# Performance work log

Measured on AMD Instinct MI355X. Metric: run time of the kernel, lower is better.

Reference implementation:

```python
import jax, jax.numpy as jnp
import numpy as np

V, H_BASE, D, L, K = 32000, 4096, 512, 2, 4
B = 64

def setup_inputs() -> dict:
    key = jax.random.key(0)
    ks = jax.random.split(key, 12)
    s = 0.02
    return {
        "hidden_state": jax.random.normal(ks[0], (B, H_BASE), jnp.float32),
        "in_proj_w": jax.random.normal(ks[1], (D, H_BASE), jnp.float32) * s,
        "in_proj_b": jnp.zeros((D,), jnp.float32),
        "w_ih0": jax.random.normal(ks[2], (3 * D, D), jnp.float32) * s,
        "w_hh0": jax.random.normal(ks[3], (3 * D, D), jnp.float32) * s,
        "b_ih0": jax.random.normal(ks[4], (3 * D,), jnp.float32) * s,
        "b_hh0": jax.random.normal(ks[5], (3 * D,), jnp.float32) * s,
        "w_ih1": jax.random.normal(ks[6], (3 * D, D), jnp.float32) * s,
        "w_hh1": jax.random.normal(ks[7], (3 * D, D), jnp.float32) * s,
        "b_ih1": jax.random.normal(ks[8], (3 * D,), jnp.float32) * s,
        "b_hh1": jax.random.normal(ks[9], (3 * D,), jnp.float32) * s,
        "embed": jax.random.normal(ks[10], (V, D), jnp.float32) * s,
        "out_w": jax.random.normal(ks[11], (V, D), jnp.float32) * s,
    }

def _gru_cell(x, h, w_ih, w_hh, b_ih, b_hh):
    # PyTorch GRU gate order: r, z, n
    gi = x @ w_ih.T + b_ih  # [B, 3D]
    gh = h @ w_hh.T + b_hh
    ir, iz, inn = jnp.split(gi, 3, axis=-1)
    hr, hz, hn = jnp.split(gh, 3, axis=-1)
    r = jax.nn.sigmoid(ir + hr)
    z = jax.nn.sigmoid(iz + hz)
    n = jnp.tanh(inn + r * hn)
    return (1.0 - z) * n + z * h

def reference(hidden_state, in_proj_w, in_proj_b, w_ih0, w_hh0, b_ih0, b_hh0,
              w_ih1, w_hh1, b_ih1, b_hh1, embed, out_w):
    b = hidden_state.shape[0]
    h0 = hidden_state @ in_proj_w.T + in_proj_b  # [B, D]
    h_l0 = h0
    h_l1 = h0
    x = jnp.zeros((b, in_proj_w.shape[0]), hidden_state.dtype)
    all_logits = []
    for _ in range(K):
        h_l0 = _gru_cell(x, h_l0, w_ih0, w_hh0, b_ih0, b_hh0)
        h_l1 = _gru_cell(h_l0, h_l1, w_ih1, w_hh1, b_ih1, b_hh1)
        logits = h_l1 @ out_w.T  # [B, V]
        all_logits.append(logits)
        x = embed[jnp.argmax(logits, axis=-1)]  # greedy next-token embed
    return jnp.stack(all_logits, axis=1)  # [B, K, V]
```

## Files before the change

kernel.cpp:

```cpp
#include <hip/hip_runtime.h>
#include <math.h>


typedef __attribute__((ext_vector_type(8))) short short8;
typedef __attribute__((ext_vector_type(4))) float f32x4;

__device__ __forceinline__ unsigned short f2bf_rne(float x) {
    unsigned u = __float_as_uint(x);
    unsigned r = (u + 0x7fffu + ((u >> 16) & 1u)) >> 16;
    return (unsigned short)r;
}
__device__ __forceinline__ void split2(float x, unsigned short& hi, unsigned short& lo) {
    unsigned u = __float_as_uint(x);
    hi = (unsigned short)(u >> 16);
    float r = x - __uint_as_float(u & 0xffff0000u);
    lo = f2bf_rne(r);
}

__device__ __forceinline__ void store_plane(unsigned short* hiP, unsigned short* loP,
                                            int m, int d, float v) {
    int s = d >> 6, cl = (d >> 3) & 7, e = d & 7;
    int off = m * 512 + s * 64 + ((cl ^ (m & 7)) * 8) + e;
    unsigned short hi, lo; split2(v, hi, lo);
    hiP[off] = hi; loP[off] = lo;
}

__device__ __forceinline__ void gload16(const void* g, void* lds) {
    __builtin_amdgcn_global_load_lds(
        (const __attribute__((address_space(1))) unsigned int*)g,
        (__attribute__((address_space(3))) unsigned int*)lds, 16, 0, 0);
}

__device__ __forceinline__ void split_w_body(
    const float* __restrict__ W, unsigned short* __restrict__ H,
    unsigned short* __restrict__ L, size_t g, int kclog)
{
    int n  = (int)(g >> kclog);
    int c8 = (int)g & ((1 << kclog) - 1);
    const float* src = W + g * 8;
    float4 v0 = *(const float4*)src;
    float4 v1 = *(const float4*)(src + 4);
    unsigned short h[8], l[8];
    split2(v0.x,h[0],l[0]); split2(v0.y,h[1],l[1]); split2(v0.z,h[2],l[2]); split2(v0.w,h[3],l[3]);
    split2(v1.x,h[4],l[4]); split2(v1.y,h[5],l[5]); split2(v1.z,h[6],l[6]); split2(v1.w,h[7],l[7]);
    uint4 ph = make_uint4((unsigned)h[0]|((unsigned)h[1]<<16), (unsigned)h[2]|((unsigned)h[3]<<16),
                          (unsigned)h[4]|((unsigned)h[5]<<16), (unsigned)h[6]|((unsigned)h[7]<<16));
    uint4 pl = make_uint4((unsigned)l[0]|((unsigned)l[1]<<16), (unsigned)l[2]|((unsigned)l[3]<<16),
                          (unsigned)l[4]|((unsigned)l[5]<<16), (unsigned)l[6]|((unsigned)l[7]<<16));
    int nt = n >> 7, row = n & 127;
    int ksi = c8 >> 3;
    int slot = (c8 & 7) ^ (row & 7);
    int tpr = 1 << (kclog - 3);
    size_t off = ((size_t)(nt * tpr + ksi) * 128 + row) * 64 + slot * 8;
    *(uint4*)(H + off) = ph;
    *(uint4*)(L + off) = pl;
}

__global__ __launch_bounds__(256) void k_split_W(
    const float* __restrict__ W, unsigned short* __restrict__ H,
    unsigned short* __restrict__ L, int kclog)
{
    size_t g = (size_t)blockIdx.x * 256 + threadIdx.x;
    split_w_body(W, H, L, g, kclog);
}

__global__ __launch_bounds__(256) void k_split_gw(
    const float* __restrict__ w0, const float* __restrict__ w1,
    const float* __restrict__ w2, const float* __restrict__ w3,
    unsigned short* __restrict__ H, unsigned short* __restrict__ L)
{
    int mat = blockIdx.y;
    const float* W = mat == 0 ? w0 : mat == 1 ? w1 : mat == 2 ? w2 : w3;
    size_t g = (size_t)blockIdx.x * 256 + threadIdx.x;
    split_w_body(W, H + (size_t)mat * 786432, L + (size_t)mat * 786432, g, 6);
}

template<bool ARGMAX>
__device__ __forceinline__ void mfma_gemm(
    const char* __restrict__ AH, const char* __restrict__ AL, int AstrideB, int akk0,
    const unsigned short* __restrict__ BH, const unsigned short* __restrict__ BL,
    size_t btileU,
    int nk,
    float* __restrict__ C, int ldc, int n0,
    unsigned short (*AsH)[4096], unsigned short (*AsL)[4096],
    unsigned short (*BsH)[8192], unsigned short (*BsL)[8192],
    float* __restrict__ pval, int* __restrict__ pidx, int bx)
{
    const int tid  = threadIdx.x;
    const int wv   = tid >> 6;
    const int lane = tid & 63;
    const int lr   = lane & 15;
    const int lh   = lane >> 4;
    const int m    = tid >> 3;
    const int cp   = tid & 7;

    f32x4 acc[4];
#pragma unroll
    for (int i = 0; i < 4; ++i) acc[i] = (f32x4){0.f, 0.f, 0.f, 0.f};

    auto stage = [&](int t, int p) {
        const int ka = (akk0 + t * 64) * 2;
        gload16(AH + m * AstrideB + ka + cp * 16, (char*)AsH[p] + wv * 1024);
        gload16(AL + m * AstrideB + ka + cp * 16, (char*)AsL[p] + wv * 1024);
        const char* bH = (const char*)BH + (btileU + (size_t)t * 8192) * 2;
        const char* bL = (const char*)BL + (btileU + (size_t)t * 8192) * 2;
        gload16(bH + wv * 2048 +        lane * 16, (char*)BsH[p] + wv * 2048);
        gload16(bH + wv * 2048 + 1024 + lane * 16, (char*)BsH[p] + wv * 2048 + 1024);
        gload16(bL + wv * 2048 +        lane * 16, (char*)BsL[p] + wv * 2048);
        gload16(bL + wv * 2048 + 1024 + lane * 16, (char*)BsL[p] + wv * 2048 + 1024);
    };

    stage(0, 0);
    __syncthreads();

    for (int t = 0; t < nk; ++t) {
        const int p = t & 1;
        if (t + 1 < nk) stage(t + 1, p ^ 1);
#pragma unroll
        for (int kk2 = 0; kk2 < 2; ++kk2) {
            int aoff = lr * 64 + (((kk2 * 4 + lh) ^ (lr & 7)) * 8);
            short8 ah[4], al[4];
#pragma unroll
            for (int mt = 0; mt < 4; ++mt) {
                ah[mt] = *(const short8*)(AsH[p] + mt * 1024 + aoff);
                al[mt] = *(const short8*)(AsL[p] + mt * 1024 + aoff);
            }
            int brow = wv * 16 + lr;
            int boff = brow * 64 + (((kk2 * 4 + lh) ^ (brow & 7)) * 8);
            short8 bh = *(const short8*)(BsH[p] + boff);
            short8 bl = *(const short8*)(BsL[p] + boff);
#pragma unroll
            for (int mt = 0; mt < 4; ++mt) {
                acc[mt] = __builtin_amdgcn_mfma_f32_16x16x32_bf16(ah[mt], bh, acc[mt], 0, 0, 0);
                acc[mt] = __builtin_amdgcn_mfma_f32_16x16x32_bf16(ah[mt], bl, acc[mt], 0, 0, 0);
                acc[mt] = __builtin_amdgcn_mfma_f32_16x16x32_bf16(al[mt], bh, acc[mt], 0, 0, 0);
            }
        }
        __syncthreads();
    }

#pragma unroll
    for (int mt = 0; mt < 4; ++mt)
#pragma unroll
        for (int i = 0; i < 4; ++i) {
            int mm = mt * 16 + lh * 4 + i;
            C[mm * ldc + n0 + wv * 16 + lr] = acc[mt][i];
        }

    if (ARGMAX) {
        float* sv = (float*)&AsH[0][0];
        int*   sc = (int*)&AsL[0][0];
#pragma unroll
        for (int mt = 0; mt < 4; ++mt)
#pragma unroll
            for (int i = 0; i < 4; ++i) {
                float v = acc[mt][i];
                int   c = n0 + wv * 16 + lr;
#pragma unroll
                for (int msk = 1; msk < 16; msk <<= 1) {
                    float ov = __shfl_xor(v, msk, 64);
                    int   oc = __shfl_xor(c, msk, 64);
                    if (ov > v || (ov == v && oc < c)) { v = ov; c = oc; }
                }
                if (lr == 0) {
                    int row = mt * 16 + lh * 4 + i;
                    sv[wv * 64 + row] = v;
                    sc[wv * 64 + row] = c;
                }
            }
        __syncthreads();
        if (tid < 64) {
            float v = sv[tid]; int c = sc[tid];
#pragma unroll
            for (int w = 1; w < 8; ++w) {
                float ov = sv[w * 64 + tid]; int oc = sc[w * 64 + tid];
                if (ov > v) { v = ov; c = oc; }
            }
            pval[bx * 64 + tid] = v;
            pidx[bx * 64 + tid] = c;
        }
    }
}

#define DECLARE_LDS() \
    __shared__ alignas(16) unsigned short AsH[2][4096]; \
    __shared__ alignas(16) unsigned short AsL[2][4096]; \
    __shared__ alignas(16) unsigned short BsH[2][8192]; \
    __shared__ alignas(16) unsigned short BsL[2][8192];

__global__ __launch_bounds__(256) void k_split_A(
    const float* __restrict__ hidden, char* __restrict__ hidH, char* __restrict__ hidL)
{
    int g = blockIdx.x * 256 + threadIdx.x;
    int m = g >> 9;
    int cc = g & 511;
    int s = cc >> 3, cl = cc & 7;
    const float* src = hidden + m * 4096 + cc * 8;
    float4 v0 = *(const float4*)src;
    float4 v1 = *(const float4*)(src + 4);
    unsigned short h[8], l[8];
    split2(v0.x,h[0],l[0]); split2(v0.y,h[1],l[1]); split2(v0.z,h[2],l[2]); split2(v0.w,h[3],l[3]);
    split2(v1.x,h[4],l[4]); split2(v1.y,h[5],l[5]); split2(v1.z,h[6],l[6]); split2(v1.w,h[7],l[7]);
    uint4 ph = make_uint4((unsigned)h[0]|((unsigned)h[1]<<16), (unsigned)h[2]|((unsigned)h[3]<<16),
                          (unsigned)h[4]|((unsigned)h[5]<<16), (unsigned)h[6]|((unsigned)h[7]<<16));
    uint4 pl = make_uint4((unsigned)l[0]|((unsigned)l[1]<<16), (unsigned)l[2]|((unsigned)l[3]<<16),
                          (unsigned)l[4]|((unsigned)l[5]<<16), (unsigned)l[6]|((unsigned)l[7]<<16));
    int off = m * 8192 + s * 128 + ((cl ^ (m & 7)) * 16);
    *(uint4*)(hidH + off) = ph;
    *(uint4*)(hidL + off) = pl;
}

__global__ __launch_bounds__(512) void k_inproj(
    const char* __restrict__ hidH, const char* __restrict__ hidL,
    const unsigned short* __restrict__ WH, const unsigned short* __restrict__ WL,
    float* __restrict__ part)
{
    DECLARE_LDS();
    int nt = blockIdx.x & 3;
    int ks = blockIdx.x >> 2;
    mfma_gemm<false>(hidH, hidL, 8192, ks * 256,
                     WH, WL, (size_t)(nt * 64 + ks * 4) * 8192, 4,
                     part + ks * 32768, 512, nt * 128,
                     AsH, AsL, BsH, BsL, nullptr, nullptr, 0);
}

__global__ __launch_bounds__(256) void k_reduce_inproj(
    const float* __restrict__ part, const float* __restrict__ bias,
    float* __restrict__ hA, float* __restrict__ hB,
    unsigned short* hAH, unsigned short* hAL,
    unsigned short* hBH, unsigned short* hBL,
    unsigned short* xH,  unsigned short* xL)
{
    int i = blockIdx.x * 256 + threadIdx.x;
    int b = i >> 9;
    int d = i & 511;
    float s = bias[d];
#pragma unroll
    for (int ks = 0; ks < 16; ++ks) s += part[ks * 32768 + i];
    hA[i] = s;
    hB[i] = s;
    store_plane(hAH, hAL, b, d, s);
    store_plane(hBH, hBL, b, d, s);
    store_plane(xH,  xL,  b, d, 0.f);
}

__global__ __launch_bounds__(512) void k_gates(
    const char* __restrict__ xH, const char* __restrict__ xL,
    const char* __restrict__ hH, const char* __restrict__ hL,
    const unsigned short* __restrict__ gwH, const unsigned short* __restrict__ gwL,
    int layer, float* __restrict__ gip, float* __restrict__ ghp)
{
    DECLARE_LDS();
    int bx  = blockIdx.x;
    int nt  = bx % 12;
    int ks  = (bx / 12) & 3;
    int mat = bx / 48;
    const char* AH = mat ? hH : xH;
    const char* AL = mat ? hL : xL;
    float* C = (mat ? ghp : gip) + ks * 98304;
    size_t btile = ((size_t)(layer * 2 + mat) * 96 + nt * 8 + ks * 2) * 8192;
    mfma_gemm<false>(AH, AL, 1024, ks * 128,
                     gwH, gwL, btile, 2,
                     C, 1536, nt * 128,
                     AsH, AsL, BsH, BsL, nullptr, nullptr, 0);
}

__global__ __launch_bounds__(256) void k_combine(
    const float* __restrict__ gip, const float* __restrict__ ghp,
    const float* __restrict__ b_ih, const float* __restrict__ b_hh,
    float* __restrict__ h, unsigned short* hH, unsigned short* hL)
{
    int i = blockIdx.x * 256 + threadIdx.x;
    int b = i >> 9;
    int d = i & 511;
    int base = b * 1536 + d;
    float ir = b_ih[d], iz = b_ih[d + 512], inn = b_ih[d + 1024];
    float hr = b_hh[d], hz = b_hh[d + 512], hn = b_hh[d + 1024];
#pragma unroll
    for (int ks = 0; ks < 4; ++ks) {
        const float* gi = gip + ks * 98304 + base;
        const float* gh = ghp + ks * 98304 + base;
        ir  += gi[0];    iz += gi[512];  inn += gi[1024];
        hr  += gh[0];    hz += gh[512];  hn  += gh[1024];
    }
    float r = 1.f / (1.f + expf(-(ir + hr)));
    float z = 1.f / (1.f + expf(-(iz + hz)));
    float n = tanhf(inn + r * hn);
    float hv = (1.f - z) * n + z * h[i];
    h[i] = hv;
    store_plane(hH, hL, b, d, hv);
}

__global__ __launch_bounds__(512) void k_logits(
    const char* __restrict__ hH, const char* __restrict__ hL,
    const unsigned short* __restrict__ WH, const unsigned short* __restrict__ WL,
    float* __restrict__ out, int step,
    float* __restrict__ pval, int* __restrict__ pidx)
{
    DECLARE_LDS();
    mfma_gemm<true>(hH, hL, 1024, 0,
                    WH, WL, (size_t)blockIdx.x * 8 * 8192, 8,
                    out + step * 32000, 128000, blockIdx.x * 128,
                    AsH, AsL, BsH, BsL, pval, pidx, blockIdx.x);
}

__global__ __launch_bounds__(256) void k_reduce_embed(
    const float* __restrict__ pval, const int* __restrict__ pidx,
    const float* __restrict__ embed, unsigned short* xH, unsigned short* xL)
{
    __shared__ float sv[256];
    __shared__ int   sc[256];
    const int b = blockIdx.x;
    const int tid = threadIdx.x;
    float v = -3.4e38f;
    int   c = 0x7fffffff;
    if (tid < 250) { v = pval[tid * 64 + b]; c = pidx[tid * 64 + b]; }
    sv[tid] = v; sc[tid] = c;
    __syncthreads();
    for (int s = 128; s > 0; s >>= 1) {
        if (tid < s) {
            float ov = sv[tid + s]; int oc = sc[tid + s];
            if (ov > sv[tid] || (ov == sv[tid] && oc < sc[tid])) { sv[tid] = ov; sc[tid] = oc; }
        }
        __syncthreads();
    }
    int tok = sc[0];
    for (int j = tid; j < 512; j += 256)
        store_plane(xH, xL, b, j, embed[tok * 512 + j]);
}

extern "C" void kernel_launch(void* const* d_in, const int* in_sizes, int n_in,
                              void* d_out, int out_size, void* d_ws, size_t ws_size,
                              hipStream_t stream)
{
    const float* hidden = (const float*)d_in[0];
    const float* in_w   = (const float*)d_in[1];
    const float* in_b   = (const float*)d_in[2];
    const float* w_ih0  = (const float*)d_in[3];
    const float* w_hh0  = (const float*)d_in[4];
    const float* b_ih0  = (const float*)d_in[5];
    const float* b_hh0  = (const float*)d_in[6];
    const float* w_ih1  = (const float*)d_in[7];
    const float* w_hh1  = (const float*)d_in[8];
    const float* b_ih1  = (const float*)d_in[9];
    const float* b_hh1  = (const float*)d_in[10];
    const float* embed  = (const float*)d_in[11];
    const float* out_w  = (const float*)d_in[12];
    float* out = (float*)d_out;
    char*  ws  = (char*)d_ws;

    float* hA  = (float*)(ws + 0);
    float* hB  = (float*)(ws + 131072);
    unsigned short* xH  = (unsigned short*)(ws + 262144);
    unsigned short* xL  = (unsigned short*)(ws + 327680);
    unsigned short* hAH = (unsigned short*)(ws + 393216);
    unsigned short* hAL = (unsigned short*)(ws + 458752);
    unsigned short* hBH = (unsigned short*)(ws + 524288);
    unsigned short* hBL = (unsigned short*)(ws + 589824);
    char* hidH = ws + 655360;
    char* hidL = ws + 1179648;
    float* gip = (float*)(ws + 1703936);
    float* ghp = (float*)(ws + 3276800);
    float* pval = (float*)(ws + 4849664);
    int*   pidx = (int*)  (ws + 4913664);
    float* ipart = (float*)(ws + 4980736);
    unsigned short* owH = (unsigned short*)(ws + 8388608);
    unsigned short* owL = (unsigned short*)(ws + 41943040);
    unsigned short* gwH = (unsigned short*)(ws + 75497472);
    unsigned short* gwL = (unsigned short*)(ws + 83886080);
    unsigned short* inH = (unsigned short*)(ws + 92274688);
    unsigned short* inL = (unsigned short*)(ws + 96468992);

    k_split_A<<<128, 256, 0, stream>>>(hidden, hidH, hidL);
    k_split_W<<<8000, 256, 0, stream>>>(out_w, owH, owL, 6);
    k_split_gw<<<dim3(384, 4), 256, 0, stream>>>(w_ih0, w_hh0, w_ih1, w_hh1, gwH, gwL);
    k_split_W<<<1024, 256, 0, stream>>>(in_w, inH, inL, 9);
    k_inproj<<<64, 512, 0, stream>>>(hidH, hidL, inH, inL, ipart);
    k_reduce_inproj<<<128, 256, 0, stream>>>(ipart, in_b, hA, hB,
                                             hAH, hAL, hBH, hBL, xH, xL);

    for (int step = 0; step < 4; ++step) {
        k_gates<<<96, 512, 0, stream>>>((char*)xH, (char*)xL, (char*)hAH, (char*)hAL,
                                        gwH, gwL, 0, gip, ghp);
        k_combine<<<128, 256, 0, stream>>>(gip, ghp, b_ih0, b_hh0, hA, hAH, hAL);
        k_gates<<<96, 512, 0, stream>>>((char*)hAH, (char*)hAL, (char*)hBH, (char*)hBL,
                                        gwH, gwL, 1, gip, ghp);
        k_combine<<<128, 256, 0, stream>>>(gip, ghp, b_ih1, b_hh1, hB, hBH, hBL);
        k_logits<<<250, 512, 0, stream>>>((char*)hBH, (char*)hBL, owH, owL,
                                          out, step, pval, pidx);
        k_reduce_embed<<<64, 256, 0, stream>>>(pval, pidx, embed, xH, xL);
    }
}
```

Before: 361.9 us.

## Fuse out_w hi/lo bf16 split into logits GEMM and drop pre-split pass

The separate kernel that split the 32000x512 fp32 out_w into bf16 hi/lo planes in workspace is removed. The logits kernel now loads fp32 out_w rows directly, splits them in registers and writes swizzled hi/lo tiles into LDS, prefetching the next tile while the current one is multiplied. Tiles shrink to 64 columns with 256 threads and 500 blocks, and the argmax partial reduction and reduce_embed are adapted to 500 partials. This removes the large write and re-read of the split planes, at the cost of repeating the split arithmetic in each of the four steps and reading fp32 (wider) weights per step.

```diff
diff --git a/kernel.cpp b/kernel.cpp
--- a/kernel.cpp
+++ b/kernel.cpp
@@ -75,119 +75,6 @@
     split_w_body(W, H + (size_t)mat * 786432, L + (size_t)mat * 786432, g, 6);
 }
 
-template<bool ARGMAX>
-__device__ __forceinline__ void mfma_gemm(
-    const char* __restrict__ AH, const char* __restrict__ AL, int AstrideB, int akk0,
-    const unsigned short* __restrict__ BH, const unsigned short* __restrict__ BL,
-    size_t btileU,
-    int nk,
-    float* __restrict__ C, int ldc, int n0,
-    unsigned short (*AsH)[4096], unsigned short (*AsL)[4096],
-    unsigned short (*BsH)[8192], unsigned short (*BsL)[8192],
-    float* __restrict__ pval, int* __restrict__ pidx, int bx)
-{
-    const int tid  = threadIdx.x;
-    const int wv   = tid >> 6;
-    const int lane = tid & 63;
-    const int lr   = lane & 15;
-    const int lh   = lane >> 4;
-    const int m    = tid >> 3;
-    const int cp   = tid & 7;
-
-    f32x4 acc[4];
-#pragma unroll
-    for (int i = 0; i < 4; ++i) acc[i] = (f32x4){0.f, 0.f, 0.f, 0.f};
-
-    auto stage = [&](int t, int p) {
-        const int ka = (akk0 + t * 64) * 2;
-        gload16(AH + m * AstrideB + ka + cp * 16, (char*)AsH[p] + wv * 1024);
-        gload16(AL + m * AstrideB + ka + cp * 16, (char*)AsL[p] + wv * 1024);
-        const char* bH = (const char*)BH + (btileU + (size_t)t * 8192) * 2;
-        const char* bL = (const char*)BL + (btileU + (size_t)t * 8192) * 2;
-        gload16(bH + wv * 2048 +        lane * 16, (char*)BsH[p] + wv * 2048);
-        gload16(bH + wv * 2048 + 1024 + lane * 16, (char*)BsH[p] + wv * 2048 + 1024);
-        gload16(bL + wv * 2048 +        lane * 16, (char*)BsL[p] + wv * 2048);
-        gload16(bL + wv * 2048 + 1024 + lane * 16, (char*)BsL[p] + wv * 2048 + 1024);
-    };
-
-    stage(0, 0);
-    __syncthreads();
-
-    for (int t = 0; t < nk; ++t) {
-        const int p = t & 1;
-        if (t + 1 < nk) stage(t + 1, p ^ 1);
-#pragma unroll
-        for (int kk2 = 0; kk2 < 2; ++kk2) {
-            int aoff = lr * 64 + (((kk2 * 4 + lh) ^ (lr & 7)) * 8);
-            short8 ah[4], al[4];
-#pragma unroll
-            for (int mt = 0; mt < 4; ++mt) {
-                ah[mt] = *(const short8*)(AsH[p] + mt * 1024 + aoff);
-                al[mt] = *(const short8*)(AsL[p] + mt * 1024 + aoff);
-            }
-            int brow = wv * 16 + lr;
-            int boff = brow * 64 + (((kk2 * 4 + lh) ^ (brow & 7)) * 8);
-            short8 bh = *(const short8*)(BsH[p] + boff);
-            short8 bl = *(const short8*)(BsL[p] + boff);
-#pragma unroll
-            for (int mt = 0; mt < 4; ++mt) {
-                acc[mt] = __builtin_amdgcn_mfma_f32_16x16x32_bf16(ah[mt], bh, acc[mt], 0, 0, 0);
-                acc[mt] = __builtin_amdgcn_mfma_f32_16x16x32_bf16(ah[mt], bl, acc[mt], 0, 0, 0);
-                acc[mt] = __builtin_amdgcn_mfma_f32_16x16x32_bf16(al[mt], bh, acc[mt], 0, 0, 0);
-            }
-        }
-        __syncthreads();
-    }
-
-#pragma unroll
-    for (int mt = 0; mt < 4; ++mt)
-#pragma unroll
-        for (int i = 0; i < 4; ++i) {
-            int mm = mt * 16 + lh * 4 + i;
-            C[mm * ldc + n0 + wv * 16 + lr] = acc[mt][i];
-        }
-
-    if (ARGMAX) {
-        float* sv = (float*)&AsH[0][0];
-        int*   sc = (int*)&AsL[0][0];
-#pragma unroll
-        for (int mt = 0; mt < 4; ++mt)
-#pragma unroll
-            for (int i = 0; i < 4; ++i) {
-                float v = acc[mt][i];
-                int   c = n0 + wv * 16 + lr;
-#pragma unroll
-                for (int msk = 1; msk < 16; msk <<= 1) {
-                    float ov = __shfl_xor(v, msk, 64);
-                    int   oc = __shfl_xor(c, msk, 64);
-                    if (ov > v || (ov == v && oc < c)) { v = ov; c = oc; }
-                }
-                if (lr == 0) {
-                    int row = mt * 16 + lh * 4 + i;
-                    sv[wv * 64 + row] = v;
-                    sc[wv * 64 + row] = c;
-                }
-            }
-        __syncthreads();
-        if (tid < 64) {
-            float v = sv[tid]; int c = sc[tid];
-#pragma unroll
-            for (int w = 1; w < 8; ++w) {
-                float ov = sv[w * 64 + tid]; int oc = sc[w * 64 + tid];
-                if (ov > v) { v = ov; c = oc; }
-            }
-            pval[bx * 64 + tid] = v;
-            pidx[bx * 64 + tid] = c;
-        }
-    }
-}
-
-#define DECLARE_LDS() \
-    __shared__ alignas(16) unsigned short AsH[2][4096]; \
-    __shared__ alignas(16) unsigned short AsL[2][4096]; \
-    __shared__ alignas(16) unsigned short BsH[2][8192]; \
-    __shared__ alignas(16) unsigned short BsL[2][8192];
-
 __global__ __launch_bounds__(256) void k_split_A(
     const float* __restrict__ hidden, char* __restrict__ hidH, char* __restrict__ hidL)
 {
@@ -210,6 +97,96 @@
     *(uint4*)(hidL + off) = pl;
 }
 
+__device__ __forceinline__ void mfma_core(
+    const unsigned short* __restrict__ AsH0, const unsigned short* __restrict__ AsL0,
+    const unsigned short* __restrict__ BsH0, const unsigned short* __restrict__ BsL0,
+    int wv, int lr, int lh, f32x4* acc)
+{
+#pragma unroll
+    for (int kk2 = 0; kk2 < 2; ++kk2) {
+        int aoff = lr * 64 + (((kk2 * 4 + lh) ^ (lr & 7)) * 8);
+        short8 ah[4], al[4];
+#pragma unroll
+        for (int mt = 0; mt < 4; ++mt) {
+            ah[mt] = *(const short8*)(AsH0 + mt * 1024 + aoff);
+            al[mt] = *(const short8*)(AsL0 + mt * 1024 + aoff);
+        }
+        int brow = wv * 16 + lr;
+        int boff = brow * 64 + (((kk2 * 4 + lh) ^ (brow & 7)) * 8);
+        short8 bh = *(const short8*)(BsH0 + boff);
+        short8 bl = *(const short8*)(BsL0 + boff);
+#pragma unroll
+        for (int mt = 0; mt < 4; ++mt) {
+            acc[mt] = __builtin_amdgcn_mfma_f32_16x16x32_bf16(ah[mt], bh, acc[mt], 0, 0, 0);
+            acc[mt] = __builtin_amdgcn_mfma_f32_16x16x32_bf16(ah[mt], bl, acc[mt], 0, 0, 0);
+            acc[mt] = __builtin_amdgcn_mfma_f32_16x16x32_bf16(al[mt], bh, acc[mt], 0, 0, 0);
+        }
+    }
+}
+
+__device__ __forceinline__ void epilogue_write(
+    float* __restrict__ C, int ldc, int n0, int wv, int lr, int lh, const f32x4* acc)
+{
+#pragma unroll
+    for (int mt = 0; mt < 4; ++mt)
+#pragma unroll
+        for (int i = 0; i < 4; ++i) {
+            int mm = mt * 16 + lh * 4 + i;
+            C[mm * ldc + n0 + wv * 16 + lr] = acc[mt][i];
+        }
+}
+
+__device__ __forceinline__ void mfma_gemm(
+    const char* __restrict__ AH, const char* __restrict__ AL, int AstrideB, int akk0,
+    const unsigned short* __restrict__ BH, const unsigned short* __restrict__ BL,
+    size_t btileU, int nk,
+    float* __restrict__ C, int ldc, int n0,
+    unsigned short (*AsH)[4096], unsigned short (*AsL)[4096],
+    unsigned short (*BsH)[8192], unsigned short (*BsL)[8192])
+{
+    const int tid  = threadIdx.x;
+    const int wv   = tid >> 6;
+    const int lane = tid & 63;
+    const int lr   = lane & 15;
+    const int lh   = lane >> 4;
+    const int m    = tid >> 3;
+    const int cp   = tid & 7;
+
+    f32x4 acc[4];
+#pragma unroll
+    for (int i = 0; i < 4; ++i) acc[i] = (f32x4){0.f, 0.f, 0.f, 0.f};
+
+    auto stage = [&](int t, int p) {
+        const int ka = (akk0 + t * 64) * 2;
+        gload16(AH + m * AstrideB + ka + cp * 16, (char*)AsH[p] + wv * 1024);
+        gload16(AL + m * AstrideB + ka + cp * 16, (char*)AsL[p] + wv * 1024);
+        const char* bH = (const char*)BH + (btileU + (size_t)t * 8192) * 2;
+        const char* bL = (const char*)BL + (btileU + (size_t)t * 8192) * 2;
+        gload16(bH + wv * 2048 +        lane * 16, (char*)BsH[p] + wv * 2048);
+        gload16(bH + wv * 2048 + 1024 + lane * 16, (char*)BsH[p] + wv * 2048 + 1024);
+        gload16(bL + wv * 2048 +        lane * 16, (char*)BsL[p] + wv * 2048);
+        gload16(bL + wv * 2048 + 1024 + lane * 16, (char*)BsL[p] + wv * 2048 + 1024);
+    };
+
+    stage(0, 0);
+    __syncthreads();
+
+    for (int t = 0; t < nk; ++t) {
+        const int p = t & 1;
+        if (t + 1 < nk) stage(t + 1, p ^ 1);
+        mfma_core(AsH[p], AsL[p], BsH[p], BsL[p], wv, lr, lh, acc);
+        __syncthreads();
+    }
+
+    epilogue_write(C, ldc, n0, wv, lr, lh, acc);
+}
+
+#define DECLARE_LDS() \
+    __shared__ alignas(16) unsigned short AsH[2][4096]; \
+    __shared__ alignas(16) unsigned short AsL[2][4096]; \
+    __shared__ alignas(16) unsigned short BsH[2][8192]; \
+    __shared__ alignas(16) unsigned short BsL[2][8192];
+
 __global__ __launch_bounds__(512) void k_inproj(
     const char* __restrict__ hidH, const char* __restrict__ hidL,
     const unsigned short* __restrict__ WH, const unsigned short* __restrict__ WL,
@@ -218,10 +195,10 @@
     DECLARE_LDS();
     int nt = blockIdx.x & 3;
     int ks = blockIdx.x >> 2;
-    mfma_gemm<false>(hidH, hidL, 8192, ks * 256,
-                     WH, WL, (size_t)(nt * 64 + ks * 4) * 8192, 4,
-                     part + ks * 32768, 512, nt * 128,
-                     AsH, AsL, BsH, BsL, nullptr, nullptr, 0);
+    mfma_gemm(hidH, hidL, 8192, ks * 256,
+              WH, WL, (size_t)(nt * 64 + ks * 4) * 8192, 4,
+              part + ks * 32768, 512, nt * 128,
+              AsH, AsL, BsH, BsL);
 }
 
 __global__ __launch_bounds__(256) void k_reduce_inproj(
@@ -259,10 +236,10 @@
     const char* AL = mat ? hL : xL;
     float* C = (mat ? ghp : gip) + ks * 98304;
     size_t btile = ((size_t)(layer * 2 + mat) * 96 + nt * 8 + ks * 2) * 8192;
-    mfma_gemm<false>(AH, AL, 1024, ks * 128,
-                     gwH, gwL, btile, 2,
-                     C, 1536, nt * 128,
-                     AsH, AsL, BsH, BsL, nullptr, nullptr, 0);
+    mfma_gemm(AH, AL, 1024, ks * 128,
+              gwH, gwL, btile, 2,
+              C, 1536, nt * 128,
+              AsH, AsL, BsH, BsL);
 }
 
 __global__ __launch_bounds__(256) void k_combine(
@@ -291,17 +268,115 @@
     store_plane(hH, hL, b, d, hv);
 }
 
-__global__ __launch_bounds__(512) void k_logits(
-    const char* __restrict__ hH, const char* __restrict__ hL,
-    const unsigned short* __restrict__ WH, const unsigned short* __restrict__ WL,
+__global__ __launch_bounds__(256) void k_logits(
+    const char* __restrict__ hBH, const char* __restrict__ hBL,
+    const float* __restrict__ out_w,
     float* __restrict__ out, int step,
     float* __restrict__ pval, int* __restrict__ pidx)
 {
-    DECLARE_LDS();
-    mfma_gemm<true>(hH, hL, 1024, 0,
-                    WH, WL, (size_t)blockIdx.x * 8 * 8192, 8,
-                    out + step * 32000, 128000, blockIdx.x * 128,
-                    AsH, AsL, BsH, BsL, pval, pidx, blockIdx.x);
+    __shared__ alignas(16) unsigned short AsH[2][4096];
+    __shared__ alignas(16) unsigned short AsL[2][4096];
+    __shared__ alignas(16) unsigned short BsH[2][4096];
+    __shared__ alignas(16) unsigned short BsL[2][4096];
+
+    const int tid  = threadIdx.x;
+    const int wv   = tid >> 6;
+    const int lane = tid & 63;
+    const int lr   = lane & 15;
+    const int lh   = lane >> 4;
+    const int bx   = blockIdx.x;
+    const int n0   = bx * 64;
+
+    const int ar1 = wv * 16 + (lane >> 3);
+    const int acp = lane & 7;
+    auto stageA = [&](int kaB, int p) {
+        gload16(hBH + ar1 * 1024 + kaB + acp * 16,       (char*)AsH[p] + wv * 2048);
+        gload16(hBH + (ar1 + 8) * 1024 + kaB + acp * 16, (char*)AsH[p] + wv * 2048 + 1024);
+        gload16(hBL + ar1 * 1024 + kaB + acp * 16,       (char*)AsL[p] + wv * 2048);
+        gload16(hBL + (ar1 + 8) * 1024 + kaB + acp * 16, (char*)AsL[p] + wv * 2048 + 1024);
+    };
+
+    const int bn = tid >> 2, bq = tid & 3;
+    const float* Wb = out_w + (size_t)(n0 + bn) * 512 + bq * 16;
+    const int wo0 = bn * 64 + (((2 * bq)     ^ (bn & 7)) * 8);
+    const int wo1 = bn * 64 + (((2 * bq + 1) ^ (bn & 7)) * 8);
+
+    float4 r0, r1, r2, r3;
+    auto loadB = [&](int t) {
+        const float* s = Wb + t * 64;
+        r0 = *(const float4*)s;       r1 = *(const float4*)(s + 4);
+        r2 = *(const float4*)(s + 8); r3 = *(const float4*)(s + 12);
+    };
+    auto writeB = [&](int p) {
+        unsigned short h[16], l[16];
+        split2(r0.x,h[0],l[0]);   split2(r0.y,h[1],l[1]);   split2(r0.z,h[2],l[2]);   split2(r0.w,h[3],l[3]);
+        split2(r1.x,h[4],l[4]);   split2(r1.y,h[5],l[5]);   split2(r1.z,h[6],l[6]);   split2(r1.w,h[7],l[7]);
+        split2(r2.x,h[8],l[8]);   split2(r2.y,h[9],l[9]);   split2(r2.z,h[10],l[10]); split2(r2.w,h[11],l[11]);
+        split2(r3.x,h[12],l[12]); split2(r3.y,h[13],l[13]); split2(r3.z,h[14],l[14]); split2(r3.w,h[15],l[15]);
+        *(uint4*)(BsH[p] + wo0) = make_uint4(
+            (unsigned)h[0]|((unsigned)h[1]<<16),  (unsigned)h[2]|((unsigned)h[3]<<16),
+            (unsigned)h[4]|((unsigned)h[5]<<16),  (unsigned)h[6]|((unsigned)h[7]<<16));
+        *(uint4*)(BsH[p] + wo1) = make_uint4(
+            (unsigned)h[8]|((unsigned)h[9]<<16),  (unsigned)h[10]|((unsigned)h[11]<<16),
+            (unsigned)h[12]|((unsigned)h[13]<<16),(unsigned)h[14]|((unsigned)h[15]<<16));
+        *(uint4*)(BsL[p] + wo0) = make_uint4(
+            (unsigned)l[0]|((unsigned)l[1]<<16),  (unsigned)l[2]|((unsigned)l[3]<<16),
+            (unsigned)l[4]|((unsigned)l[5]<<16),  (unsigned)l[6]|((unsigned)l[7]<<16));
+        *(uint4*)(BsL[p] + wo1) = make_uint4(
+            (unsigned)l[8]|((unsigned)l[9]<<16),  (unsigned)l[10]|((unsigned)l[11]<<16),
+            (unsigned)l[12]|((unsigned)l[13]<<16),(unsigned)l[14]|((unsigned)l[15]<<16));
+    };
+
+    f32x4 acc[4];
+#pragma unroll
+    for (int i = 0; i < 4; ++i) acc[i] = (f32x4){0.f, 0.f, 0.f, 0.f};
+
+    loadB(0);
+    stageA(0, 0);
+    writeB(0);
+    __syncthreads();
+#pragma unroll
+    for (int t = 0; t < 8; ++t) {
+        const int p = t & 1;
+        if (t < 7) { loadB(t + 1); stageA((t + 1) * 128, p ^ 1); }
+        mfma_core(AsH[p], AsL[p], BsH[p], BsL[p], wv, lr, lh, acc);
+        if (t < 7) writeB(p ^ 1);
+        __syncthreads();
+    }
+
+    epilogue_write(out + step * 32000, 128000, n0, wv, lr, lh, acc);
+
+    float* sv = (float*)&AsH[0][0];
+    int*   sc = (int*)&AsL[0][0];
+#pragma unroll
+    for (int mt = 0; mt < 4; ++mt)
+#pragma unroll
+        for (int i = 0; i < 4; ++i) {
+            float v = acc[mt][i];
+            int   c = n0 + wv * 16 + lr;
+#pragma unroll
+            for (int msk = 1; msk < 16; msk <<= 1) {
+                float ov = __shfl_xor(v, msk, 64);
+                int   oc = __shfl_xor(c, msk, 64);
+                if (ov > v || (ov == v && oc < c)) { v = ov; c = oc; }
+            }
+            if (lr == 0) {
+                int row = mt * 16 + lh * 4 + i;
+                sv[wv * 64 + row] = v;
+                sc[wv * 64 + row] = c;
+            }
+        }
+    __syncthreads();
+    if (tid < 64) {
+        float v = sv[tid]; int c = sc[tid];
+#pragma unroll
+        for (int w = 1; w < 4; ++w) {
+            float ov = sv[w * 64 + tid]; int oc = sc[w * 64 + tid];
+            if (ov > v || (ov == v && oc < c)) { v = ov; c = oc; }
+        }
+        pval[bx * 64 + tid] = v;
+        pidx[bx * 64 + tid] = c;
+    }
 }
 
 __global__ __launch_bounds__(256) void k_reduce_embed(
@@ -312,9 +387,13 @@
     __shared__ int   sc[256];
     const int b = blockIdx.x;
     const int tid = threadIdx.x;
-    float v = -3.4e38f;
-    int   c = 0x7fffffff;
-    if (tid < 250) { v = pval[tid * 64 + b]; c = pidx[tid * 64 + b]; }
+    float v = pval[tid * 64 + b];
+    int   c = pidx[tid * 64 + b];
+    if (tid + 256 < 500) {
+        float ov = pval[(tid + 256) * 64 + b];
+        int   oc = pidx[(tid + 256) * 64 + b];
+        if (ov > v || (ov == v && oc < c)) { v = ov; c = oc; }
+    }
     sv[tid] = v; sc[tid] = c;
     __syncthreads();
     for (int s = 128; s > 0; s >>= 1) {
@@ -326,7 +405,7 @@
     }
     int tok = sc[0];
     for (int j = tid; j < 512; j += 256)
-        store_plane(xH, xL, b, j, embed[tok * 512 + j]);
+        store_plane(xH, xL, b, j, embed[(size_t)tok * 512 + j]);
 }
 
 extern "C" void kernel_launch(void* const* d_in, const int* in_sizes, int n_in,
@@ -362,17 +441,14 @@
     float* gip = (float*)(ws + 1703936);
     float* ghp = (float*)(ws + 3276800);
     float* pval = (float*)(ws + 4849664);
-    int*   pidx = (int*)  (ws + 4913664);
-    float* ipart = (float*)(ws + 4980736);
-    unsigned short* owH = (unsigned short*)(ws + 8388608);
-    unsigned short* owL = (unsigned short*)(ws + 41943040);
-    unsigned short* gwH = (unsigned short*)(ws + 75497472);
-    unsigned short* gwL = (unsigned short*)(ws + 83886080);
-    unsigned short* inH = (unsigned short*)(ws + 92274688);
-    unsigned short* inL = (unsigned short*)(ws + 96468992);
+    int*   pidx = (int*)  (ws + 4980736);
+    float* ipart = (float*)(ws + 5111808);
+    unsigned short* gwH = (unsigned short*)(ws + 7208960);
+    unsigned short* gwL = (unsigned short*)(ws + 13500416);
+    unsigned short* inH = (unsigned short*)(ws + 19791872);
+    unsigned short* inL = (unsigned short*)(ws + 23986176);
 
     k_split_A<<<128, 256, 0, stream>>>(hidden, hidH, hidL);
-    k_split_W<<<8000, 256, 0, stream>>>(out_w, owH, owL, 6);
     k_split_gw<<<dim3(384, 4), 256, 0, stream>>>(w_ih0, w_hh0, w_ih1, w_hh1, gwH, gwL);
     k_split_W<<<1024, 256, 0, stream>>>(in_w, inH, inL, 9);
     k_inproj<<<64, 512, 0, stream>>>(hidH, hidL, inH, inL, ipart);
@@ -386,7 +462,7 @@
         k_gates<<<96, 512, 0, stream>>>((char*)hAH, (char*)hAL, (char*)hBH, (char*)hBL,
                                         gwH, gwL, 1, gip, ghp);
         k_combine<<<128, 256, 0, stream>>>(gip, ghp, b_ih1, b_hh1, hB, hBH, hBL);
-        k_logits<<<250, 512, 0, stream>>>((char*)hBH, (char*)hBL, owH, owL,
+        k_logits<<<500, 256, 0, stream>>>((char*)hBH, (char*)hBL, out_w,
                                           out, step, pval, pidx);
         k_reduce_embed<<<64, 256, 0, stream>>>(pval, pidx, embed, xH, xL);
     }
```

Result: no change. 357.8 us (-1.1%).
